# Kernel tuning notes

Measured on AMD Instinct MI355X. Metric: run time of the kernel, lower is better.

The kernel has to match this reference:

```python
import jax, jax.numpy as jnp
import numpy as np
import math

B, H, N, D = 2, 16, 2048, 128
SM_SCALE = 1.0 / math.sqrt(D)


def setup_inputs() -> dict:
    key = jax.random.key(0)
    kq, kk, kv = jax.random.split(key, 3)
    q = jax.random.normal(kq, (B, H, N, D), dtype=jnp.float32)
    k = jax.random.normal(kk, (B, H, N, D), dtype=jnp.float32)
    v = jax.random.normal(kv, (B, H, N, D), dtype=jnp.float32)
    return {"q": q, "k": k, "v": v}


def reference(q, k, v):
    # RBF-kernel causal attention (non-softmax):
    #   logits_ij = -sm_scale * ||q_i - k_j||^2
    #            = 2*sm_scale*q_i.k_j - sm_scale*||q_i||^2 - sm_scale*||k_j||^2
    #   p = exp(logits) with causal mask (p_ij = 0 for j > i); out = p @ v
    sm_scale = jnp.float32(SM_SCALE)
    q_sq = sm_scale * jnp.sum(q * q, axis=-1)  # [B,H,N]
    k_sq = sm_scale * jnp.sum(k * k, axis=-1)  # [B,H,N]
    qk = jnp.einsum("bhmd,bhnd->bhmn", q, k)
    logits = (2.0 * sm_scale) * qk - q_sq[..., :, None] - k_sq[..., None, :]
    n = q.shape[2]
    causal = jnp.tril(jnp.ones((n, n), dtype=bool))
    logits = jnp.where(causal, logits, -jnp.inf)
    p = jnp.exp(logits)  # NOT normalized (non-softmax attention)
    out = jnp.einsum("bhmn,bhnd->bhmd", p, v)
    return out
```

## Files before the change

kernel.cpp:

```cpp
#include <hip/hip_runtime.h>
#include <math.h>


#define NSEQ 2048
#define DH   128
#define BHC  32
#define SM_SCALE 0.08838834764831845f

typedef __attribute__((ext_vector_type(8))) short    short8;
typedef __attribute__((ext_vector_type(8))) _Float16 half8;
typedef __attribute__((ext_vector_type(4))) short    short4_;
typedef __attribute__((ext_vector_type(4))) float    float4_;
typedef __attribute__((ext_vector_type(4))) unsigned uint4_;
typedef __attribute__((ext_vector_type(2))) unsigned uint2_;

#define KST 136
#define VST 72

__device__ __forceinline__ short f2bf(float x){
  union{float f; unsigned u;} a; a.f=x;
  unsigned r = a.u + 0x7fffu + ((a.u>>16)&1u);
  return (short)(r>>16);
}
__device__ __forceinline__ float bf2f(short h){
  union{float f; unsigned u;} a; a.u=((unsigned)(unsigned short)h)<<16; return a.f;
}
__device__ __forceinline__ unsigned packbf(float a, float b){
  return (unsigned)(unsigned short)f2bf(a) | ((unsigned)(unsigned short)f2bf(b)<<16);
}
__device__ __forceinline__ unsigned cvtpk_bf16(float a, float b){
  unsigned r;
  asm("v_cvt_pk_bf16_f32 %0, %1, %2" : "=v"(r) : "v"(a), "v"(b));
  return r;
}

__device__ __forceinline__ void qswap32(unsigned A, unsigned B, unsigned &X, unsigned &Y){
  uint2_ r = __builtin_amdgcn_permlane32_swap(A, B, false, false);
  X = r[0]; Y = r[1];
}
__device__ __forceinline__ void qswap16(unsigned A, unsigned B, unsigned &X, unsigned &Y, int oddq){
#if __has_builtin(__builtin_amdgcn_permlane16_swap)
  uint2_ r = __builtin_amdgcn_permlane16_swap(A, B, false, false);
  X = r[0]; Y = r[1];
#else
  unsigned As = (unsigned)__builtin_amdgcn_ds_swizzle((int)A, 0x401F);
  unsigned Bs = (unsigned)__builtin_amdgcn_ds_swizzle((int)B, 0x401F);
  X = oddq ? Bs : A;
  Y = oddq ? B  : As;
#endif
}

__global__ __launch_bounds__(256)
void prep_kv5(const float* __restrict__ kg, const float* __restrict__ vg,
              _Float16* __restrict__ khg, short* __restrict__ vtg,
              float* __restrict__ ksqg){
  __shared__ unsigned Vls[128*33];
  const int b = blockIdx.x, t = threadIdx.x;
  const int l = t & 63, wv = t >> 6;
  if(b < 1024){
    const int bh = b>>5, jt = b&31;
    const float4_* vb4 = (const float4_*)(vg + ((size_t)bh*NSEQ + (size_t)jt*64)*DH);
    #pragma unroll
    for(int i=0;i<8;++i){
      float4_ own = vb4[i*256 + t];
      float4_ par;
      par.x = __shfl_xor(own.x, 32); par.y = __shfl_xor(own.y, 32);
      par.z = __shfl_xor(own.z, 32); par.w = __shfl_xor(own.w, 32);
      const int hi = (l>>5)&1;
      unsigned w0 = hi ? packbf(par.z, own.z) : packbf(own.x, par.x);
      unsigned w1 = hi ? packbf(par.w, own.w) : packbf(own.y, par.y);
      const int dd = 4*(t&31) + 2*hi;
      const int j2 = 4*i + wv;
      Vls[dd*33 + j2]     = w0;
      Vls[(dd+1)*33 + j2] = w1;
    }
    __syncthreads();
    short* outp = vtg + ((size_t)(bh*32 + jt)*DH)*64;
    #pragma unroll
    for(int it=0; it<4; ++it){
      int idx = t + 256*it;
      int d = idx>>3, slot = idx&7;
      uint4_ o;
      o.x = Vls[d*33 + 4*slot];   o.y = Vls[d*33 + 4*slot+1];
      o.z = Vls[d*33 + 4*slot+2]; o.w = Vls[d*33 + 4*slot+3];
      *(uint4_*)(outp + d*64 + 8*slot) = o;
    }
  } else {
    const int kb = b - 1024;
    const float4_* kb4 = (const float4_*)(kg + (size_t)kb*64*DH);
    #pragma unroll
    for(int i=0;i<8;++i){
      float4_ x = kb4[i*256 + t];
      const int row = 64*kb + 8*i + (t>>5);
      const int d   = 4*(t&31);
      union{ _Float16 h[4]; uint2_ u; } pk;
      pk.h[0]=(_Float16)x.x; pk.h[1]=(_Float16)x.y;
      pk.h[2]=(_Float16)x.z; pk.h[3]=(_Float16)x.w;
      *(uint2_*)(khg + (size_t)row*DH + d) = pk.u;
      float ss = x.x*x.x + x.y*x.y + x.z*x.z + x.w*x.w;
      ss += __shfl_xor(ss,1);  ss += __shfl_xor(ss,2);
      ss += __shfl_xor(ss,4);  ss += __shfl_xor(ss,8);
      ss += __shfl_xor(ss,16);
      if((l&31)==0) ksqg[row] = SM_SCALE*ss;
    }
  }
}

__global__ __launch_bounds__(256,2)
void rbf_attn9(const float* __restrict__ qg,
               const _Float16* __restrict__ khg,
               const short* __restrict__ vtg,
               const float* __restrict__ ksqg,
               float* __restrict__ og){
  __shared__ short Kst[64*KST];
  __shared__ short Vst[128*VST];
  __shared__ float ksLs[64];

  const int tid=threadIdx.x;
  const int w=tid>>6, l=tid&63;
  const int quad=l>>4, lr=l&15;
  const int bh=blockIdx.x;
  const int y = blockIdx.y;
  const int g = y>>3, z = y&7;
  const int mq = g*8 + ((g&1) ? (7-z) : z);
  const int qbase = 64*mq + 16*w;

  const float*    Qg = qg   + (size_t)bh*NSEQ*DH;
  const _Float16* Kh = khg  + (size_t)bh*NSEQ*DH;
  const short*    Vt = vtg  + (size_t)bh*32*DH*64;
  const float*    Ks = ksqg + (size_t)bh*NSEQ;
  float*          Og = og   + (size_t)bh*NSEQ*DH;

  half8 qf[4];
  float qsq;
  {
    const int qrow = qbase + lr;
    const float* qp = Qg + (size_t)qrow*DH + 8*quad;
    float ss=0.f;
    #pragma unroll
    for(int ks=0;ks<4;++ks){
      float4_ a = *(const float4_*)(qp + 32*ks);
      float4_ b = *(const float4_*)(qp + 32*ks + 4);
      half8 h;
      #pragma unroll
      for(int j=0;j<4;++j){
        h[j]   = (_Float16)a[j];
        h[j+4] = (_Float16)b[j];
        ss += a[j]*a[j] + b[j]*b[j];
      }
      qf[ks]=h;
    }
    ss += __shfl_xor(ss,16);
    ss += __shfl_xor(ss,32);
    qsq = SM_SCALE*ss;
  }

  float4_ oacc[8];
  #pragma unroll
  for(int b2=0;b2<8;++b2) oacc[b2] = (float4_)0.f;

  uint4_ kreg[4], vreg[4];
  float  kqreg = 0.f;
  {
    #pragma unroll
    for(int it=0;it<4;++it){
      int idx = tid + 256*it;
      int row = idx>>4, c = idx&15;
      kreg[it] = *(const uint4_*)(Kh + (size_t)row*DH + 8*c);
      int d = idx>>3, slot = idx&7;
      vreg[it] = *(const uint4_*)(Vt + (size_t)d*64 + 8*slot);
    }
    if(tid<64) kqreg = Ks[tid];
  }

  for(int jt=0; jt<=mq; ++jt){
    #pragma unroll
    for(int it=0;it<4;++it){
      int idx = tid + 256*it;
      int row = idx>>4, c = idx&15;
      *(uint4_*)&Kst[row*KST + 8*c] = kreg[it];
      int d = idx>>3, slot = idx&7;
      *(uint4_*)&Vst[d*VST + 8*slot] = vreg[it];
    }
    if(tid<64) ksLs[tid] = kqreg;
    __syncthreads();

    if(jt < mq){
      const int jc2 = (jt+1)*64;
      #pragma unroll
      for(int it=0;it<4;++it){
        int idx = tid + 256*it;
        int row = idx>>4, c = idx&15;
        kreg[it] = *(const uint4_*)(Kh + (size_t)(jc2+row)*DH + 8*c);
        int d = idx>>3, slot = idx&7;
        vreg[it] = *(const uint4_*)(Vt + ((size_t)(jt+1)*DH + d)*64 + 8*slot);
      }
      if(tid<64) kqreg = Ks[jc2 + tid];
    }

    const bool diag = (jt == mq);
    const int ctmax = diag ? w : 3;
    const int nks2  = (diag && w < 2) ? 1 : 2;

    float4_ sacc[4];
    #pragma unroll
    for(int ct=0;ct<4;++ct) sacc[ct] = (float4_)0.f;

    __builtin_amdgcn_s_setprio(1);
    #pragma unroll
    for(int ks=0;ks<4;++ks){
      half8 kf[4];
      #pragma unroll
      for(int ct=0;ct<4;++ct)
        if(ct<=ctmax) kf[ct] = *(const half8*)&Kst[(16*ct+lr)*KST + 32*ks + 8*quad];
      #pragma unroll
      for(int ct=0;ct<4;++ct)
        if(ct<=ctmax) sacc[ct]=__builtin_amdgcn_mfma_f32_16x16x32_f16(kf[ct],qf[ks],sacc[ct],0,0,0);
    }
    __builtin_amdgcn_s_setprio(0);

    unsigned pk[4][2];
    {
      const int jg0 = 64*jt;
      const int qrow = qbase + lr;
      #pragma unroll
      for(int ct=0;ct<4;++ct){
        if(ct < 2*nks2){
          float4_ kq = *(const float4_*)&ksLs[16*ct + 4*quad];
          const int j0 = jg0 + 16*ct + 4*quad;
          float p[4];
          #pragma unroll
          for(int r=0;r<4;++r){
            float logit = (2.f*SM_SCALE)*sacc[ct][r] - qsq - kq[r];
            p[r] = (j0 + r <= qrow) ? __expf(logit) : 0.f;
          }
          pk[ct][0] = cvtpk_bf16(p[0], p[1]);
          pk[ct][1] = cvtpk_bf16(p[2], p[3]);
        }
      }
    }

    __builtin_amdgcn_s_setprio(1);
    #pragma unroll
    for(int ks2=0;ks2<2;++ks2){
      if(ks2 < nks2){
        unsigned A0,B0,A1,B1;
        qswap32(pk[2*ks2][0], pk[2*ks2+1][0], A0, B0);
        qswap32(pk[2*ks2][1], pk[2*ks2+1][1], A1, B1);
        unsigned w0,w1,w2,w3;
        qswap16(A0, B0, w0, w2, quad&1);
        qswap16(A1, B1, w1, w3, quad&1);
        union{ uint4_ u; short8 s; } pfu;
        pfu.u.x=w0; pfu.u.y=w1; pfu.u.z=w2; pfu.u.w=w3;
        const short8 pf = pfu.s;
        #pragma unroll
        for(int ctv=0;ctv<8;++ctv){
          const short8 vf = *(const short8*)&Vst[(16*ctv+lr)*VST + 32*ks2 + 8*quad];
          oacc[ctv]=__builtin_amdgcn_mfma_f32_16x16x32_bf16(pf,vf,oacc[ctv],0,0,0);
        }
      }
    }
    __builtin_amdgcn_s_setprio(0);

    __syncthreads();
  }

  #pragma unroll
  for(int ctv=0;ctv<8;++ctv)
    #pragma unroll
    for(int r=0;r<4;++r){
      const int qrow = qbase + 4*quad + r;
      Og[(size_t)qrow*DH + 16*ctv + lr] = oacc[ctv][r];
    }
}

#define KSTf 136
#define VSTf 36
#define PSTf 72

__global__ __launch_bounds__(256,2)
void rbf_attn_mfma(const float* __restrict__ qg, const float* __restrict__ kg,
                   const float* __restrict__ vg, float* __restrict__ og){
  __shared__ short    Khi[64*KSTf];
  __shared__ short    Klo[64*KSTf];
  __shared__ unsigned VP [128*VSTf];
  __shared__ short    Pfb[64*PSTf];
  __shared__ float    qsq_s[64];
  __shared__ float    ksq_s[64];

  const int tid=threadIdx.x;
  const int w=tid>>6, l=tid&63;
  const int wr=w>>1, wc=w&1;
  const int quad=l>>4, lr=l&15;
  const int bh=blockIdx.x, yp=blockIdx.y;

  const float* Qg = qg + (size_t)bh*NSEQ*DH;
  const float* Kg = kg + (size_t)bh*NSEQ*DH;
  const float* Vg = vg + (size_t)bh*NSEQ*DH;
  float*       Og = og + (size_t)bh*NSEQ*DH;

  for(int pass=0;pass<2;++pass){
    const int m = pass ? (31-yp) : yp;
    __syncthreads();
    short8 qhf[2][4], qlf[2][4];
    #pragma unroll
    for(int rt=0;rt<2;++rt){
      const int grow = m*64 + 32*wr + 16*rt + lr;
      const float* qp = Qg + (size_t)grow*DH + 8*quad;
      float ss=0.f;
      #pragma unroll
      for(int ks=0;ks<4;++ks){
        float4_ a = *(const float4_*)(qp + 32*ks);
        float4_ b = *(const float4_*)(qp + 32*ks + 4);
        short8 hi, lo;
        #pragma unroll
        for(int j=0;j<4;++j){
          float fa=a[j], fb=b[j];
          short ha=f2bf(fa); hi[j]=ha;   lo[j]=f2bf(fa-bf2f(ha));
          short hb=f2bf(fb); hi[j+4]=hb; lo[j+4]=f2bf(fb-bf2f(hb));
          ss += fa*fa + fb*fb;
        }
        qhf[rt][ks]=hi; qlf[rt][ks]=lo;
      }
      ss += __shfl_xor(ss,16);
      ss += __shfl_xor(ss,32);
      if(wc==0 && quad==0) qsq_s[32*wr+16*rt+lr] = SM_SCALE*ss;
    }
    float4_ oacc[2][4];
    #pragma unroll
    for(int a=0;a<2;++a)
      #pragma unroll
      for(int b=0;b<4;++b) oacc[a][b] = (float4_)0.f;

    const int ntiles = m+1;
    for(int jt=0;jt<ntiles;++jt){
      const int jc = jt*64;
      __syncthreads();
      #pragma unroll
      for(int it=0;it<4;++it){
        const int i = tid + 256*it;
        const int row = i>>4, c0 = 8*(i&15);
        const float* kp = Kg + (size_t)(jc+row)*DH + c0;
        float4_ a = *(const float4_*)kp;
        float4_ b = *(const float4_*)(kp+4);
        short8 hi, lo;
        float ss=0.f;
        #pragma unroll
        for(int j=0;j<4;++j){
          float fa=a[j], fb=b[j];
          short ha=f2bf(fa); hi[j]=ha;   lo[j]=f2bf(fa-bf2f(ha));
          short hb=f2bf(fb); hi[j+4]=hb; lo[j+4]=f2bf(fb-bf2f(hb));
          ss += fa*fa + fb*fb;
        }
        ss += __shfl_xor(ss,1); ss += __shfl_xor(ss,2);
        ss += __shfl_xor(ss,4); ss += __shfl_xor(ss,8);
        if(lr==0) ksq_s[row] = SM_SCALE*ss;
        *(short8*)&Khi[row*KSTf + c0] = hi;
        *(short8*)&Klo[row*KSTf + c0] = lo;
      }
      #pragma unroll
      for(int it=0;it<4;++it){
        const int u = tid + 256*it;
        const int d = u & 127, jg = u >> 7;
        const float* vp = Vg + (size_t)(jc + 8*jg)*DH + d;
        float vv[8];
        #pragma unroll
        for(int jj=0;jj<8;++jj) vv[jj] = vp[(size_t)jj*DH];
        uint4_ pk;
        #pragma unroll
        for(int p2=0;p2<4;++p2)
          pk[p2] = (unsigned)(unsigned short)f2bf(vv[2*p2]) |
                   ((unsigned)(unsigned short)f2bf(vv[2*p2+1])<<16);
        *(uint4_*)&VP[d*VSTf + 4*jg] = pk;
      }
      __syncthreads();
      float4_ sacc[2][2];
      #pragma unroll
      for(int a=0;a<2;++a)
        #pragma unroll
        for(int b=0;b<2;++b) sacc[a][b] = (float4_)0.f;
      #pragma unroll
      for(int ks=0;ks<4;++ks){
        short8 khf[2], klf[2];
        #pragma unroll
        for(int ct=0;ct<2;++ct){
          const int off = (32*wc + 16*ct + lr)*KSTf + 32*ks + 8*quad;
          khf[ct] = *(const short8*)&Khi[off];
          klf[ct] = *(const short8*)&Klo[off];
        }
        #pragma unroll
        for(int rt=0;rt<2;++rt)
          #pragma unroll
          for(int ct=0;ct<2;++ct){
            sacc[rt][ct]=__builtin_amdgcn_mfma_f32_16x16x32_bf16(qhf[rt][ks],khf[ct],sacc[rt][ct],0,0,0);
            sacc[rt][ct]=__builtin_amdgcn_mfma_f32_16x16x32_bf16(qhf[rt][ks],klf[ct],sacc[rt][ct],0,0,0);
            sacc[rt][ct]=__builtin_amdgcn_mfma_f32_16x16x32_bf16(qlf[rt][ks],khf[ct],sacc[rt][ct],0,0,0);
          }
      }
      #pragma unroll
      for(int rt=0;rt<2;++rt){
        float qs[4];
        #pragma unroll
        for(int r=0;r<4;++r) qs[r]=qsq_s[32*wr+16*rt+4*quad+r];
        #pragma unroll
        for(int ct=0;ct<2;++ct){
          const float ksq = ksq_s[32*wc+16*ct+lr];
          const int colg = jc + 32*wc+16*ct+lr;
          #pragma unroll
          for(int r=0;r<4;++r){
            const int rowg = m*64 + 32*wr+16*rt+4*quad+r;
            float logit = (2.f*SM_SCALE)*sacc[rt][ct][r] - qs[r] - ksq;
            float p = (colg<=rowg)? __expf(logit) : 0.f;
            Pfb[(32*wr+16*rt+4*quad+r)*PSTf + 32*wc+16*ct+lr] = f2bf(p);
          }
        }
      }
      __syncthreads();
      #pragma unroll
      for(int ks2=0;ks2<2;++ks2){
        short8 pf[2];
        #pragma unroll
        for(int rt=0;rt<2;++rt)
          pf[rt] = *(const short8*)&Pfb[(32*wr+16*rt+lr)*PSTf + 32*ks2 + 8*quad];
        #pragma unroll
        for(int ctv=0;ctv<4;++ctv){
          const int d = 64*wc + 16*ctv + lr;
          const short8 vfb = *(const short8*)((const short*)VP + d*(2*VSTf) + 32*ks2 + 8*quad);
          #pragma unroll
          for(int rt=0;rt<2;++rt)
            oacc[rt][ctv]=__builtin_amdgcn_mfma_f32_16x16x32_bf16(pf[rt],vfb,oacc[rt][ctv],0,0,0);
        }
      }
    }
    #pragma unroll
    for(int rt=0;rt<2;++rt)
      #pragma unroll
      for(int ctv=0;ctv<4;++ctv)
        #pragma unroll
        for(int r=0;r<4;++r){
          const int rowg = m*64 + 32*wr + 16*rt + 4*quad + r;
          Og[(size_t)rowg*DH + 64*wc + 16*ctv + lr] = oacc[rt][ctv][r];
        }
  }
}

extern "C" void kernel_launch(void* const* d_in, const int* in_sizes, int n_in,
                              void* d_out, int out_size, void* d_ws, size_t ws_size,
                              hipStream_t stream) {
  const float* q = (const float*)d_in[0];
  const float* k = (const float*)d_in[1];
  const float* v = (const float*)d_in[2];
  float* out = (float*)d_out;

  const size_t nElem = (size_t)BHC*NSEQ*DH;
  const size_t need  = nElem*2*sizeof(short) + (size_t)BHC*NSEQ*sizeof(float);

  if(ws_size >= need){
    _Float16* khg = (_Float16*)d_ws;
    short*    vtg = (short*)(khg + nElem);
    float*    ksqg = (float*)(vtg + nElem);
    prep_kv5<<<2048, 256, 0, stream>>>(k, v, khg, vtg, ksqg);
    rbf_attn9<<<dim3(BHC,32), 256, 0, stream>>>(q, khg, vtg, ksqg, out);
  } else {
    rbf_attn_mfma<<<dim3(BHC,16), 256, 0, stream>>>(q, k, v, out);
  }
}
```

Baseline: 201.6 us.

## Double Q tile per block to 128 rows with double-buffered K/V LDS

Each block now processes 128 query rows, with each wave owning two 16-row tiles, so every K/V tile loaded into LDS feeds twice as many MFMAs. K/V shared buffers are double-buffered, which drops one barrier per iteration. The grid is halved to 16 y-blocks, paired so that short and long causal rows balance. The costs are more registers for the doubled accumulators, higher LDS use and the loss of the 2-blocks-per-CU launch bound, which may lower occupancy. There is also more causal-tail waste on diagonal tiles.

```diff
diff --git a/kernel.cpp b/kernel.cpp
--- a/kernel.cpp
+++ b/kernel.cpp
@@ -106,24 +106,24 @@
   }
 }
 
-__global__ __launch_bounds__(256,2)
-void rbf_attn9(const float* __restrict__ qg,
-               const _Float16* __restrict__ khg,
-               const short* __restrict__ vtg,
-               const float* __restrict__ ksqg,
-               float* __restrict__ og){
-  __shared__ short Kst[64*KST];
-  __shared__ short Vst[128*VST];
-  __shared__ float ksLs[64];
+__global__ __launch_bounds__(256)
+void rbf_attn10(const float* __restrict__ qg,
+                const _Float16* __restrict__ khg,
+                const short* __restrict__ vtg,
+                const float* __restrict__ ksqg,
+                float* __restrict__ og){
+  __shared__ short Kst[2][64*KST];
+  __shared__ short Vst[2][128*VST];
+  __shared__ float ksLs[2][64];
 
   const int tid=threadIdx.x;
   const int w=tid>>6, l=tid&63;
   const int quad=l>>4, lr=l&15;
   const int bh=blockIdx.x;
   const int y = blockIdx.y;
-  const int g = y>>3, z = y&7;
-  const int mq = g*8 + ((g&1) ? (7-z) : z);
-  const int qbase = 64*mq + 16*w;
+  const int t = (y<8) ? y : 23-y;
+  const int qbase = 128*t + 32*w;
+  const int jtmax = 2*t+1;
 
   const float*    Qg = qg   + (size_t)bh*NSEQ*DH;
   const _Float16* Kh = khg  + (size_t)bh*NSEQ*DH;
@@ -131,10 +131,11 @@
   const float*    Ks = ksqg + (size_t)bh*NSEQ;
   float*          Og = og   + (size_t)bh*NSEQ*DH;
 
-  half8 qf[4];
-  float qsq;
-  {
-    const int qrow = qbase + lr;
+  half8 qf[2][4];
+  float qsq[2];
+  #pragma unroll
+  for(int rt=0;rt<2;++rt){
+    const int qrow = qbase + 16*rt + lr;
     const float* qp = Qg + (size_t)qrow*DH + 8*quad;
     float ss=0.f;
     #pragma unroll
@@ -148,16 +149,18 @@
         h[j+4] = (_Float16)b[j];
         ss += a[j]*a[j] + b[j]*b[j];
       }
-      qf[ks]=h;
+      qf[rt][ks]=h;
     }
     ss += __shfl_xor(ss,16);
     ss += __shfl_xor(ss,32);
-    qsq = SM_SCALE*ss;
-  }
-
-  float4_ oacc[8];
+    qsq[rt] = SM_SCALE*ss;
+  }
+
+  float4_ oacc[2][8];
   #pragma unroll
-  for(int b2=0;b2<8;++b2) oacc[b2] = (float4_)0.f;
+  for(int a=0;a<2;++a)
+    #pragma unroll
+    for(int b2=0;b2<8;++b2) oacc[a][b2] = (float4_)0.f;
 
   uint4_ kreg[4], vreg[4];
   float  kqreg = 0.f;
@@ -172,20 +175,23 @@
     }
     if(tid<64) kqreg = Ks[tid];
   }
-
-  for(int jt=0; jt<=mq; ++jt){
+  {
     #pragma unroll
     for(int it=0;it<4;++it){
       int idx = tid + 256*it;
       int row = idx>>4, c = idx&15;
-      *(uint4_*)&Kst[row*KST + 8*c] = kreg[it];
+      *(uint4_*)&Kst[0][row*KST + 8*c] = kreg[it];
       int d = idx>>3, slot = idx&7;
-      *(uint4_*)&Vst[d*VST + 8*slot] = vreg[it];
-    }
-    if(tid<64) ksLs[tid] = kqreg;
+      *(uint4_*)&Vst[0][d*VST + 8*slot] = vreg[it];
+    }
+    if(tid<64) ksLs[0][tid] = kqreg;
+  }
+
+  int cur = 0;
+  for(int jt=0; jt<=jtmax; ++jt){
     __syncthreads();
 
-    if(jt < mq){
+    if(jt < jtmax){
       const int jc2 = (jt+1)*64;
       #pragma unroll
       for(int it=0;it<4;++it){
@@ -198,80 +204,110 @@
       if(tid<64) kqreg = Ks[jc2 + tid];
     }
 
-    const bool diag = (jt == mq);
-    const int ctmax = diag ? w : 3;
-    const int nks2  = (diag && w < 2) ? 1 : 2;
-
-    float4_ sacc[4];
-    #pragma unroll
-    for(int ct=0;ct<4;++ct) sacc[ct] = (float4_)0.f;
-
-    __builtin_amdgcn_s_setprio(1);
-    #pragma unroll
-    for(int ks=0;ks<4;++ks){
-      half8 kf[4];
-      #pragma unroll
-      for(int ct=0;ct<4;++ct)
-        if(ct<=ctmax) kf[ct] = *(const half8*)&Kst[(16*ct+lr)*KST + 32*ks + 8*quad];
-      #pragma unroll
-      for(int ct=0;ct<4;++ct)
-        if(ct<=ctmax) sacc[ct]=__builtin_amdgcn_mfma_f32_16x16x32_f16(kf[ct],qf[ks],sacc[ct],0,0,0);
-    }
-    __builtin_amdgcn_s_setprio(0);
-
-    unsigned pk[4][2];
-    {
-      const int jg0 = 64*jt;
-      const int qrow = qbase + lr;
-      #pragma unroll
-      for(int ct=0;ct<4;++ct){
-        if(ct < 2*nks2){
-          float4_ kq = *(const float4_*)&ksLs[16*ct + 4*quad];
-          const int j0 = jg0 + 16*ct + 4*quad;
-          float p[4];
+    const int rel = qbase + 31 - 64*jt;
+    if(rel >= 0){
+      const int ctmax = (rel>>4) < 3 ? (rel>>4) : 3;
+      const int nks2  = (rel >= 32) ? 2 : 1;
+
+      float4_ sacc[2][4];
+      #pragma unroll
+      for(int a=0;a<2;++a)
+        #pragma unroll
+        for(int ct=0;ct<4;++ct) sacc[a][ct] = (float4_)0.f;
+
+      __builtin_amdgcn_s_setprio(1);
+      #pragma unroll
+      for(int ks=0;ks<4;++ks){
+        half8 kf[4];
+        #pragma unroll
+        for(int ct=0;ct<4;++ct)
+          if(ct<=ctmax) kf[ct] = *(const half8*)&Kst[cur][(16*ct+lr)*KST + 32*ks + 8*quad];
+        #pragma unroll
+        for(int ct=0;ct<4;++ct)
+          if(ct<=ctmax){
+            sacc[0][ct]=__builtin_amdgcn_mfma_f32_16x16x32_f16(kf[ct],qf[0][ks],sacc[0][ct],0,0,0);
+            sacc[1][ct]=__builtin_amdgcn_mfma_f32_16x16x32_f16(kf[ct],qf[1][ks],sacc[1][ct],0,0,0);
+          }
+      }
+      __builtin_amdgcn_s_setprio(0);
+
+      unsigned pk[2][4][2];
+      {
+        const int jg0 = 64*jt;
+        #pragma unroll
+        for(int rt=0;rt<2;++rt){
+          const int qrow = qbase + 16*rt + lr;
+          const float qs = qsq[rt];
           #pragma unroll
-          for(int r=0;r<4;++r){
-            float logit = (2.f*SM_SCALE)*sacc[ct][r] - qsq - kq[r];
-            p[r] = (j0 + r <= qrow) ? __expf(logit) : 0.f;
+          for(int ct=0;ct<4;++ct){
+            if(ct < 2*nks2){
+              float4_ kq = *(const float4_*)&ksLs[cur][16*ct + 4*quad];
+              const int j0 = jg0 + 16*ct + 4*quad;
+              float p[4];
+              #pragma unroll
+              for(int r=0;r<4;++r){
+                float logit = (2.f*SM_SCALE)*sacc[rt][ct][r] - qs - kq[r];
+                p[r] = (j0 + r <= qrow) ? __expf(logit) : 0.f;
+              }
+              pk[rt][ct][0] = cvtpk_bf16(p[0], p[1]);
+              pk[rt][ct][1] = cvtpk_bf16(p[2], p[3]);
+            }
           }
-          pk[ct][0] = cvtpk_bf16(p[0], p[1]);
-          pk[ct][1] = cvtpk_bf16(p[2], p[3]);
-        }
-      }
-    }
-
-    __builtin_amdgcn_s_setprio(1);
-    #pragma unroll
-    for(int ks2=0;ks2<2;++ks2){
-      if(ks2 < nks2){
-        unsigned A0,B0,A1,B1;
-        qswap32(pk[2*ks2][0], pk[2*ks2+1][0], A0, B0);
-        qswap32(pk[2*ks2][1], pk[2*ks2+1][1], A1, B1);
-        unsigned w0,w1,w2,w3;
-        qswap16(A0, B0, w0, w2, quad&1);
-        qswap16(A1, B1, w1, w3, quad&1);
-        union{ uint4_ u; short8 s; } pfu;
-        pfu.u.x=w0; pfu.u.y=w1; pfu.u.z=w2; pfu.u.w=w3;
-        const short8 pf = pfu.s;
-        #pragma unroll
-        for(int ctv=0;ctv<8;++ctv){
-          const short8 vf = *(const short8*)&Vst[(16*ctv+lr)*VST + 32*ks2 + 8*quad];
-          oacc[ctv]=__builtin_amdgcn_mfma_f32_16x16x32_bf16(pf,vf,oacc[ctv],0,0,0);
-        }
-      }
-    }
-    __builtin_amdgcn_s_setprio(0);
-
-    __syncthreads();
+        }
+      }
+
+      __builtin_amdgcn_s_setprio(1);
+      #pragma unroll
+      for(int ks2=0;ks2<2;++ks2){
+        if(ks2 < nks2){
+          short8 pf[2];
+          #pragma unroll
+          for(int rt=0;rt<2;++rt){
+            unsigned A0,B0,A1,B1;
+            qswap32(pk[rt][2*ks2][0], pk[rt][2*ks2+1][0], A0, B0);
+            qswap32(pk[rt][2*ks2][1], pk[rt][2*ks2+1][1], A1, B1);
+            unsigned w0,w1,w2,w3;
+            qswap16(A0, B0, w0, w2, quad&1);
+            qswap16(A1, B1, w1, w3, quad&1);
+            union{ uint4_ u; short8 s; } pfu;
+            pfu.u.x=w0; pfu.u.y=w1; pfu.u.z=w2; pfu.u.w=w3;
+            pf[rt] = pfu.s;
+          }
+          #pragma unroll
+          for(int ctv=0;ctv<8;++ctv){
+            const short8 vf = *(const short8*)&Vst[cur][(16*ctv+lr)*VST + 32*ks2 + 8*quad];
+            oacc[0][ctv]=__builtin_amdgcn_mfma_f32_16x16x32_bf16(pf[0],vf,oacc[0][ctv],0,0,0);
+            oacc[1][ctv]=__builtin_amdgcn_mfma_f32_16x16x32_bf16(pf[1],vf,oacc[1][ctv],0,0,0);
+          }
+        }
+      }
+      __builtin_amdgcn_s_setprio(0);
+    }
+
+    if(jt < jtmax){
+      const int nxt = cur^1;
+      #pragma unroll
+      for(int it=0;it<4;++it){
+        int idx = tid + 256*it;
+        int row = idx>>4, c = idx&15;
+        *(uint4_*)&Kst[nxt][row*KST + 8*c] = kreg[it];
+        int d = idx>>3, slot = idx&7;
+        *(uint4_*)&Vst[nxt][d*VST + 8*slot] = vreg[it];
+      }
+      if(tid<64) ksLs[nxt][tid] = kqreg;
+    }
+    cur ^= 1;
   }
 
   #pragma unroll
-  for(int ctv=0;ctv<8;++ctv)
-    #pragma unroll
-    for(int r=0;r<4;++r){
-      const int qrow = qbase + 4*quad + r;
-      Og[(size_t)qrow*DH + 16*ctv + lr] = oacc[ctv][r];
-    }
+  for(int rt=0;rt<2;++rt)
+    #pragma unroll
+    for(int ctv=0;ctv<8;++ctv)
+      #pragma unroll
+      for(int r=0;r<4;++r){
+        const int qrow = qbase + 16*rt + 4*quad + r;
+        Og[(size_t)qrow*DH + 16*ctv + lr] = oacc[rt][ctv][r];
+      }
 }
 
 #define KSTf 136
@@ -460,7 +496,7 @@
     short*    vtg = (short*)(khg + nElem);
     float*    ksqg = (float*)(vtg + nElem);
     prep_kv5<<<2048, 256, 0, stream>>>(k, v, khg, vtg, ksqg);
-    rbf_attn9<<<dim3(BHC,32), 256, 0, stream>>>(q, khg, vtg, ksqg, out);
+    rbf_attn10<<<dim3(BHC,16), 256, 0, stream>>>(q, khg, vtg, ksqg, out);
   } else {
     rbf_attn_mfma<<<dim3(BHC,16), 256, 0, stream>>>(q, k, v, out);
   }
```

Result: no change. 205.0 us (+1.7%).
